# Optimization experiments

Hardware: AMD Instinct MI355X
Metric: run time of the kernel (lower is better)

Reference implementation:

```python
import jax, jax.numpy as jnp
import numpy as np

EPS = 1e-6

def setup_inputs() -> dict:
    key = jax.random.key(0)
    k1, k2 = jax.random.split(key)
    n, c, h, w = 16, 256, 64, 64
    n_F = w
    X = jax.random.normal(k1, (n, c, h, w), dtype=jnp.float32)
    # xavier_uniform for W [n_F, n_F]
    limit = float(np.sqrt(6.0 / (n_F + n_F)))
    W = jax.random.uniform(k2, (n_F, n_F), dtype=jnp.float32, minval=-limit, maxval=limit)
    a2 = jnp.ones((n_F,), dtype=jnp.float32)
    b2 = jnp.zeros((n_F,), dtype=jnp.float32)
    return {"X": X, "W": W, "a2": a2, "b2": b2}

def reference(X, W, a2, b2):
    n, c, h, w = X.shape
    Xf = X.reshape(n * c, h, w)                      # [nc, h, w]
    # attention-like matrix: transpose then softmax over last axis (length h)
    A = jax.nn.softmax(jnp.swapaxes(Xf, 1, 2), axis=2)  # [nc, w, h]
    # custom LayerNorm with unbiased std (torch x.std default, ddof=1)
    mean = jnp.mean(Xf, axis=-1, keepdims=True)
    std = jnp.std(Xf, axis=-1, ddof=1, keepdims=True)
    Xn = a2 * (Xf - mean) / (std + EPS) + b2          # [nc, h, w]
    node = jnp.matmul(A, Xn)                          # [nc, w, w]
    out = jax.nn.relu(jnp.matmul(node, W))            # [nc, w, w]
    return out.reshape(n, c, h, w)
```

## Files before the change

kernel.cpp:

```cpp
#include <hip/hip_runtime.h>


typedef __attribute__((ext_vector_type(8)))  short  s16x8;
typedef __attribute__((ext_vector_type(16))) float  f32x16;
typedef __attribute__((ext_vector_type(8)))  unsigned short us8;

__device__ __forceinline__ unsigned short f2bf(float x) {
    unsigned u = __builtin_bit_cast(unsigned, x);
    u += 0x7FFFu + ((u >> 16) & 1u);
    return (unsigned short)(u >> 16);
}
__device__ __forceinline__ float bf2f(unsigned short h) {
    unsigned u = ((unsigned)h) << 16;
    return __builtin_bit_cast(float, u);
}
__device__ __forceinline__ int swidx(int row, int k) {
    return row * 64 + (k ^ ((row & 7) << 3));
}

__global__ __launch_bounds__(256, 3)
void gnn_mfma(const float* __restrict__ X, const float* __restrict__ Wg,
              const float* __restrict__ a2, const float* __restrict__ b2,
              float* __restrict__ out)
{
    __shared__ __align__(16) unsigned short bufA[2][64 * 64];
    __shared__ __align__(16) unsigned short bufX[2][64 * 64];
    __shared__ __align__(16) unsigned short bufW[2][64 * 64];

    const int tid = threadIdx.x;
    const int b   = blockIdx.x;
    const float* xb = X + (size_t)b * 4096;

    {
        const int wi = tid >> 2;
        const int h0 = (tid & 3) << 4;
        float v[16];
        #pragma unroll
        for (int i = 0; i < 16; ++i) v[i] = xb[(h0 + i) * 64 + wi];
        float m = v[0];
        #pragma unroll
        for (int i = 1; i < 16; ++i) m = fmaxf(m, v[i]);
        m = fmaxf(m, __shfl_xor(m, 1));
        m = fmaxf(m, __shfl_xor(m, 2));
        float s = 0.f;
        #pragma unroll
        for (int i = 0; i < 16; ++i) { v[i] = __expf(v[i] - m); s += v[i]; }
        s += __shfl_xor(s, 1);
        s += __shfl_xor(s, 2);
        const float inv = 1.0f / s;
        us8 hv0, lv0, hv1, lv1;
        #pragma unroll
        for (int i = 0; i < 8; ++i) {
            float p = v[i] * inv;
            unsigned short hh = f2bf(p);
            hv0[i] = hh; lv0[i] = f2bf(p - bf2f(hh));
        }
        #pragma unroll
        for (int i = 0; i < 8; ++i) {
            float p = v[8 + i] * inv;
            unsigned short hh = f2bf(p);
            hv1[i] = hh; lv1[i] = f2bf(p - bf2f(hh));
        }
        const int sw = (wi & 7) << 3;
        const int i0 = wi * 64 + (h0 ^ sw);
        const int i1 = wi * 64 + ((h0 + 8) ^ sw);
        *(us8*)&bufA[0][i0] = hv0; *(us8*)&bufA[0][i1] = hv1;
        *(us8*)&bufA[1][i0] = lv0; *(us8*)&bufA[1][i1] = lv1;
    }

    {
        const int h  = tid >> 2;
        const int c0 = (tid & 3) << 4;
        float x[16];
        #pragma unroll
        for (int i = 0; i < 4; ++i) {
            float4 t = *(const float4*)&xb[h * 64 + c0 + 4 * i];
            x[4 * i] = t.x; x[4 * i + 1] = t.y; x[4 * i + 2] = t.z; x[4 * i + 3] = t.w;
        }
        float s = 0.f, sq = 0.f;
        #pragma unroll
        for (int i = 0; i < 16; ++i) { s += x[i]; sq += x[i] * x[i]; }
        s  += __shfl_xor(s, 1);  s  += __shfl_xor(s, 2);
        sq += __shfl_xor(sq, 1); sq += __shfl_xor(sq, 2);
        const float mean = s * (1.0f / 64.0f);
        float var = (sq - 64.0f * mean * mean) * (1.0f / 63.0f);
        var = fmaxf(var, 0.0f);
        const float invstd = 1.0f / (sqrtf(var) + 1e-6f);
        float av[16], bv[16];
        #pragma unroll
        for (int i = 0; i < 4; ++i) {
            float4 ta = *(const float4*)&a2[c0 + 4 * i];
            float4 tb = *(const float4*)&b2[c0 + 4 * i];
            av[4*i] = ta.x; av[4*i+1] = ta.y; av[4*i+2] = ta.z; av[4*i+3] = ta.w;
            bv[4*i] = tb.x; bv[4*i+1] = tb.y; bv[4*i+2] = tb.z; bv[4*i+3] = tb.w;
        }
        #pragma unroll
        for (int i = 0; i < 16; ++i) {
            float xn = av[i] * (x[i] - mean) * invstd + bv[i];
            unsigned short hh = f2bf(xn);
            const int idx = swidx(c0 + i, h);
            bufX[0][idx] = hh;
            bufX[1][idx] = f2bf(xn - bf2f(hh));
        }
    }

    {
        const int j = tid & 63;
        const int q = tid >> 6;
        float wv[16];
        #pragma unroll
        for (int i = 0; i < 16; ++i) wv[i] = Wg[(16 * q + i) * 64 + j];
        us8 hv0, lv0, hv1, lv1;
        #pragma unroll
        for (int i = 0; i < 8; ++i) {
            unsigned short hh = f2bf(wv[i]);
            hv0[i] = hh; lv0[i] = f2bf(wv[i] - bf2f(hh));
        }
        #pragma unroll
        for (int i = 0; i < 8; ++i) {
            unsigned short hh = f2bf(wv[8 + i]);
            hv1[i] = hh; lv1[i] = f2bf(wv[8 + i] - bf2f(hh));
        }
        const int sw = (j & 7) << 3;
        const int i0 = j * 64 + ((16 * q) ^ sw);
        const int i1 = j * 64 + ((16 * q + 8) ^ sw);
        *(us8*)&bufW[0][i0] = hv0; *(us8*)&bufW[0][i1] = hv1;
        *(us8*)&bufW[1][i0] = lv0; *(us8*)&bufW[1][i1] = lv1;
    }
    __syncthreads();

    const int wid  = tid >> 6;
    const int lane = tid & 63;
    const int r    = lane & 31;
    const int hl   = lane >> 5;
    const int R = (wid & 1) * 32;
    const int C = (wid >> 1) * 32;

    f32x16 acc;
    #pragma unroll
    for (int i = 0; i < 16; ++i) acc[i] = 0.f;

    const int rowA = R + r;
    const int rowB = C + r;
    #pragma unroll
    for (int t = 0; t < 4; ++t) {
        const int k0 = 16 * t + 8 * hl;
        s16x8 aH = *(const s16x8*)&bufA[0][rowA * 64 + (k0 ^ ((rowA & 7) << 3))];
        s16x8 aL = *(const s16x8*)&bufA[1][rowA * 64 + (k0 ^ ((rowA & 7) << 3))];
        s16x8 bH = *(const s16x8*)&bufX[0][rowB * 64 + (k0 ^ ((rowB & 7) << 3))];
        s16x8 bL = *(const s16x8*)&bufX[1][rowB * 64 + (k0 ^ ((rowB & 7) << 3))];
        acc = __builtin_amdgcn_mfma_f32_32x32x16_bf16(aH, bH, acc, 0, 0, 0);
        acc = __builtin_amdgcn_mfma_f32_32x32x16_bf16(aH, bL, acc, 0, 0, 0);
        acc = __builtin_amdgcn_mfma_f32_32x32x16_bf16(aL, bH, acc, 0, 0, 0);
    }
    __syncthreads();

    #pragma unroll
    for (int g = 0; g < 16; ++g) {
        const int w1 = R + (g & 3) + 8 * (g >> 2) + 4 * hl;
        const float xv = acc[g];
        const unsigned short hh = f2bf(xv);
        const int idx = swidx(w1, C + r);
        bufA[0][idx] = hh;
        bufA[1][idx] = f2bf(xv - bf2f(hh));
    }
    __syncthreads();

    f32x16 acc2;
    #pragma unroll
    for (int i = 0; i < 16; ++i) acc2[i] = 0.f;

    const int rowN = R + r;
    const int rowW = C + r;
    #pragma unroll
    for (int t = 0; t < 4; ++t) {
        const int k0 = 16 * t + 8 * hl;
        s16x8 nH = *(const s16x8*)&bufA[0][rowN * 64 + (k0 ^ ((rowN & 7) << 3))];
        s16x8 nL = *(const s16x8*)&bufA[1][rowN * 64 + (k0 ^ ((rowN & 7) << 3))];
        s16x8 wH = *(const s16x8*)&bufW[0][rowW * 64 + (k0 ^ ((rowW & 7) << 3))];
        s16x8 wL = *(const s16x8*)&bufW[1][rowW * 64 + (k0 ^ ((rowW & 7) << 3))];
        acc2 = __builtin_amdgcn_mfma_f32_32x32x16_bf16(nH, wH, acc2, 0, 0, 0);
        acc2 = __builtin_amdgcn_mfma_f32_32x32x16_bf16(nH, wL, acc2, 0, 0, 0);
        acc2 = __builtin_amdgcn_mfma_f32_32x32x16_bf16(nL, wH, acc2, 0, 0, 0);
    }

    float* ob = out + (size_t)b * 4096;
    #pragma unroll
    for (int g = 0; g < 16; ++g) {
        const int w1 = R + (g & 3) + 8 * (g >> 2) + 4 * hl;
        ob[w1 * 64 + C + r] = fmaxf(acc2[g], 0.f);
    }
}

extern "C" void kernel_launch(void* const* d_in, const int* in_sizes, int n_in,
                              void* d_out, int out_size, void* d_ws, size_t ws_size,
                              hipStream_t stream) {
    const float* X  = (const float*)d_in[0];
    const float* W  = (const float*)d_in[1];
    const float* a2 = (const float*)d_in[2];
    const float* b2 = (const float*)d_in[3];
    float* out = (float*)d_out;
    gnn_mfma<<<4096, 256, 0, stream>>>(X, W, a2, b2, out);
}
```

Measured before the change: 136.6 us.

## Precompute split-bf16 W in a prep kernel, drop low part of softmax, shrink LDS

Adds a small prep kernel that converts W once into swizzled hi/lo bf16 planes in workspace, which each block then copies straight into LDS instead of doing a strided load and split per block. The softmax matrix is stored only as a single bf16 (its low-part MFMA is dropped), which removes one LDS buffer, raises the occupancy hint from 3 to 4 blocks, and reuses bufX for the low part of the intermediate. It also switches to a two-level XOR swizzle and uses the HIP bf16 conversion intrinsic. The cost is lower precision in the A·Xn product and an extra kernel launch.

After: 131.2 us. 3.9% less time.

```diff
diff --git a/kernel.cpp b/kernel.cpp
--- a/kernel.cpp
+++ b/kernel.cpp
@@ -1,4 +1,5 @@
 #include <hip/hip_runtime.h>
+#include <hip/hip_bf16.h>
 
 
 typedef __attribute__((ext_vector_type(8)))  short  s16x8;
@@ -6,30 +7,54 @@
 typedef __attribute__((ext_vector_type(8)))  unsigned short us8;
 
 __device__ __forceinline__ unsigned short f2bf(float x) {
-    unsigned u = __builtin_bit_cast(unsigned, x);
-    u += 0x7FFFu + ((u >> 16) & 1u);
-    return (unsigned short)(u >> 16);
+    __hip_bfloat16 b = __float2bfloat16(x);
+    return __builtin_bit_cast(unsigned short, b);
 }
 __device__ __forceinline__ float bf2f(unsigned short h) {
     unsigned u = ((unsigned)h) << 16;
     return __builtin_bit_cast(float, u);
 }
+__device__ __forceinline__ int swz(int row) {
+    return ((row & 7) ^ ((row >> 3) & 7)) << 3;
+}
 __device__ __forceinline__ int swidx(int row, int k) {
-    return row * 64 + (k ^ ((row & 7) << 3));
+    return row * 64 + (k ^ swz(row));
 }
 
-__global__ __launch_bounds__(256, 3)
-void gnn_mfma(const float* __restrict__ X, const float* __restrict__ Wg,
+__global__ void prep_w(const float* __restrict__ Wg, unsigned short* __restrict__ ws) {
+    const int gid = blockIdx.x * 256 + threadIdx.x;
+    const int j = gid & 63;
+    const int k = gid >> 6;
+    const float x = Wg[k * 64 + j];
+    const unsigned short hh = f2bf(x);
+    const unsigned short ll = f2bf(x - bf2f(hh));
+    const int idx = swidx(j, k);
+    ws[idx] = hh;
+    ws[4096 + idx] = ll;
+}
+
+__global__ __launch_bounds__(256, 4)
+void gnn_mfma(const float* __restrict__ X, const unsigned short* __restrict__ Wp,
               const float* __restrict__ a2, const float* __restrict__ b2,
               float* __restrict__ out)
 {
-    __shared__ __align__(16) unsigned short bufA[2][64 * 64];
+    __shared__ __align__(16) unsigned short bufA[64 * 64];
     __shared__ __align__(16) unsigned short bufX[2][64 * 64];
     __shared__ __align__(16) unsigned short bufW[2][64 * 64];
 
     const int tid = threadIdx.x;
     const int b   = blockIdx.x;
     const float* xb = X + (size_t)b * 4096;
+
+    {
+        const us8* src = (const us8*)Wp;
+        us8* dh = (us8*)bufW[0];
+        us8* dl = (us8*)bufW[1];
+        dh[2 * tid]     = src[2 * tid];
+        dh[2 * tid + 1] = src[2 * tid + 1];
+        dl[2 * tid]     = src[512 + 2 * tid];
+        dl[2 * tid + 1] = src[512 + 2 * tid + 1];
+    }
 
     {
         const int wi = tid >> 2;
@@ -48,24 +73,14 @@
         s += __shfl_xor(s, 1);
         s += __shfl_xor(s, 2);
         const float inv = 1.0f / s;
-        us8 hv0, lv0, hv1, lv1;
+        us8 hv0, hv1;
         #pragma unroll
-        for (int i = 0; i < 8; ++i) {
-            float p = v[i] * inv;
-            unsigned short hh = f2bf(p);
-            hv0[i] = hh; lv0[i] = f2bf(p - bf2f(hh));
-        }
+        for (int i = 0; i < 8; ++i) hv0[i] = f2bf(v[i] * inv);
         #pragma unroll
-        for (int i = 0; i < 8; ++i) {
-            float p = v[8 + i] * inv;
-            unsigned short hh = f2bf(p);
-            hv1[i] = hh; lv1[i] = f2bf(p - bf2f(hh));
-        }
-        const int sw = (wi & 7) << 3;
-        const int i0 = wi * 64 + (h0 ^ sw);
-        const int i1 = wi * 64 + ((h0 + 8) ^ sw);
-        *(us8*)&bufA[0][i0] = hv0; *(us8*)&bufA[0][i1] = hv1;
-        *(us8*)&bufA[1][i0] = lv0; *(us8*)&bufA[1][i1] = lv1;
+        for (int i = 0; i < 8; ++i) hv1[i] = f2bf(v[8 + i] * inv);
+        const int sw = swz(wi);
+        *(us8*)&bufA[wi * 64 + (h0 ^ sw)]       = hv0;
+        *(us8*)&bufA[wi * 64 + ((h0 + 8) ^ sw)] = hv1;
     }
 
     {
@@ -96,36 +111,12 @@
         }
         #pragma unroll
         for (int i = 0; i < 16; ++i) {
-            float xn = av[i] * (x[i] - mean) * invstd + bv[i];
-            unsigned short hh = f2bf(xn);
+            const float xn = av[i] * (x[i] - mean) * invstd + bv[i];
+            const unsigned short hh = f2bf(xn);
             const int idx = swidx(c0 + i, h);
             bufX[0][idx] = hh;
             bufX[1][idx] = f2bf(xn - bf2f(hh));
         }
-    }
-
-    {
-        const int j = tid & 63;
-        const int q = tid >> 6;
-        float wv[16];
-        #pragma unroll
-        for (int i = 0; i < 16; ++i) wv[i] = Wg[(16 * q + i) * 64 + j];
-        us8 hv0, lv0, hv1, lv1;
-        #pragma unroll
-        for (int i = 0; i < 8; ++i) {
-            unsigned short hh = f2bf(wv[i]);
-            hv0[i] = hh; lv0[i] = f2bf(wv[i] - bf2f(hh));
-        }
-        #pragma unroll
-        for (int i = 0; i < 8; ++i) {
-            unsigned short hh = f2bf(wv[8 + i]);
-            hv1[i] = hh; lv1[i] = f2bf(wv[8 + i] - bf2f(hh));
-        }
-        const int sw = (j & 7) << 3;
-        const int i0 = j * 64 + ((16 * q) ^ sw);
-        const int i1 = j * 64 + ((16 * q + 8) ^ sw);
-        *(us8*)&bufW[0][i0] = hv0; *(us8*)&bufW[0][i1] = hv1;
-        *(us8*)&bufW[1][i0] = lv0; *(us8*)&bufW[1][i1] = lv1;
     }
     __syncthreads();
 
@@ -136,22 +127,23 @@
     const int R = (wid & 1) * 32;
     const int C = (wid >> 1) * 32;
 
+    const int rowA = R + r;
+    const int rowB = C + r;
+    const int swA = swz(rowA);
+    const int swB = swz(rowB);
+
     f32x16 acc;
     #pragma unroll
     for (int i = 0; i < 16; ++i) acc[i] = 0.f;
 
-    const int rowA = R + r;
-    const int rowB = C + r;
     #pragma unroll
     for (int t = 0; t < 4; ++t) {
         const int k0 = 16 * t + 8 * hl;
-        s16x8 aH = *(const s16x8*)&bufA[0][rowA * 64 + (k0 ^ ((rowA & 7) << 3))];
-        s16x8 aL = *(const s16x8*)&bufA[1][rowA * 64 + (k0 ^ ((rowA & 7) << 3))];
-        s16x8 bH = *(const s16x8*)&bufX[0][rowB * 64 + (k0 ^ ((rowB & 7) << 3))];
-        s16x8 bL = *(const s16x8*)&bufX[1][rowB * 64 + (k0 ^ ((rowB & 7) << 3))];
+        s16x8 aH = *(const s16x8*)&bufA[rowA * 64 + (k0 ^ swA)];
+        s16x8 bH = *(const s16x8*)&bufX[0][rowB * 64 + (k0 ^ swB)];
+        s16x8 bL = *(const s16x8*)&bufX[1][rowB * 64 + (k0 ^ swB)];
         acc = __builtin_amdgcn_mfma_f32_32x32x16_bf16(aH, bH, acc, 0, 0, 0);
         acc = __builtin_amdgcn_mfma_f32_32x32x16_bf16(aH, bL, acc, 0, 0, 0);
-        acc = __builtin_amdgcn_mfma_f32_32x32x16_bf16(aL, bH, acc, 0, 0, 0);
     }
     __syncthreads();
 
@@ -161,8 +153,8 @@
         const float xv = acc[g];
         const unsigned short hh = f2bf(xv);
         const int idx = swidx(w1, C + r);
-        bufA[0][idx] = hh;
-        bufA[1][idx] = f2bf(xv - bf2f(hh));
+        bufA[idx]    = hh;
+        bufX[0][idx] = f2bf(xv - bf2f(hh));
     }
     __syncthreads();
 
@@ -170,15 +162,13 @@
     #pragma unroll
     for (int i = 0; i < 16; ++i) acc2[i] = 0.f;
 
-    const int rowN = R + r;
-    const int rowW = C + r;
     #pragma unroll
     for (int t = 0; t < 4; ++t) {
         const int k0 = 16 * t + 8 * hl;
-        s16x8 nH = *(const s16x8*)&bufA[0][rowN * 64 + (k0 ^ ((rowN & 7) << 3))];
-        s16x8 nL = *(const s16x8*)&bufA[1][rowN * 64 + (k0 ^ ((rowN & 7) << 3))];
-        s16x8 wH = *(const s16x8*)&bufW[0][rowW * 64 + (k0 ^ ((rowW & 7) << 3))];
-        s16x8 wL = *(const s16x8*)&bufW[1][rowW * 64 + (k0 ^ ((rowW & 7) << 3))];
+        s16x8 nH = *(const s16x8*)&bufA[rowA * 64 + (k0 ^ swA)];
+        s16x8 nL = *(const s16x8*)&bufX[0][rowA * 64 + (k0 ^ swA)];
+        s16x8 wH = *(const s16x8*)&bufW[0][rowB * 64 + (k0 ^ swB)];
+        s16x8 wL = *(const s16x8*)&bufW[1][rowB * 64 + (k0 ^ swB)];
         acc2 = __builtin_amdgcn_mfma_f32_32x32x16_bf16(nH, wH, acc2, 0, 0, 0);
         acc2 = __builtin_amdgcn_mfma_f32_32x32x16_bf16(nH, wL, acc2, 0, 0, 0);
         acc2 = __builtin_amdgcn_mfma_f32_32x32x16_bf16(nL, wH, acc2, 0, 0, 0);
@@ -200,5 +190,7 @@
     const float* a2 = (const float*)d_in[2];
     const float* b2 = (const float*)d_in[3];
     float* out = (float*)d_out;
-    gnn_mfma<<<4096, 256, 0, stream>>>(X, W, a2, b2, out);
+    unsigned short* wp = (unsigned short*)d_ws;
+    prep_w<<<16, 256, 0, stream>>>(W, wp);
+    gnn_mfma<<<4096, 256, 0, stream>>>(X, wp, a2, b2, out);
 }
```
